# Kernel tuning notes

Measured on AMD Instinct MI355X. Metric: run time of the kernel, lower is better.

Reference implementation:

```python
import jax, jax.numpy as jnp
import numpy as np

N_NODES = 50000
N_EDGES = 800000
D_IN = 96
D_EDGE = 32
D_OUT = 96
N_TYPES = 4


def setup_inputs() -> dict:
    key = jax.random.key(0)
    k = jax.random.split(key, 6)
    x = jax.random.normal(k[0], (N_NODES, D_IN), dtype=jnp.float32)
    edge_features = jax.random.normal(k[1], (N_NODES, D_EDGE), dtype=jnp.float32)
    edge_index = jax.random.randint(k[2], (2, N_EDGES), 0, N_NODES, dtype=jnp.int32)
    edge_type = jax.random.randint(k[3], (N_EDGES,), 0, N_TYPES, dtype=jnp.int32)
    # One RelEdgeConv per relation type: Linear(D_IN + D_EDGE -> D_OUT) message fn
    scale = 1.0 / np.sqrt(D_IN + D_EDGE)
    W_msg = jax.random.uniform(k[4], (N_TYPES, D_IN + D_EDGE, D_OUT), jnp.float32, -scale, scale)
    b_msg = jax.random.uniform(k[5], (N_TYPES, D_OUT), jnp.float32, -scale, scale)
    return {"x": x, "edge_features": edge_features, "edge_index": edge_index,
            "edge_type": edge_type, "W_msg": W_msg, "b_msg": b_msg}


def reference(x, edge_features, edge_index, edge_type, W_msg, b_msg):
    # Node-level edge_features (shape[0] == N) -> per-edge relative features
    src, dst = edge_index[0], edge_index[1]
    e = jnp.abs(edge_features[src] - edge_features[dst])          # [E, De]
    feat = jnp.concatenate([x[src], e], axis=-1)                  # [E, Din+De]
    n_nodes = x.shape[0]
    n_types = W_msg.shape[0]

    def per_type(t):
        # relation mask: zero out messages for edges of other types
        mask = (edge_type == t).astype(x.dtype)[:, None]          # [E, 1]
        m = (feat @ W_msg[t] + b_msg[t]) * mask                   # [E, Dout]
        # scatter-add messages to destination nodes
        return jax.ops.segment_sum(m, dst, num_segments=n_nodes)  # [N, Dout]

    out = jnp.stack([per_type(t) for t in range(n_types)])        # [T, N, Dout]
    return out.mean(axis=0)
```

## Files before the change

kernel.cpp:

```cpp
#include <hip/hip_runtime.h>

#define E_EDGES 800000
#define NN 50000
#define D_IN 96
#define D_EDGE 32
#define D_OUT 96
#define KSUM 512
#define SSTRIDE 520
#define NBUCK 196
#define BCAP 4800
#define NCHUNK 256
#define CHE 3125
#define CHIT 13
#define BUILD_BLOCKS 512
#define SUBCAP 384

typedef __attribute__((ext_vector_type(8))) __bf16 bf16x8;
typedef __attribute__((ext_vector_type(4))) float floatx4;

__device__ __forceinline__ float lo16(unsigned int u) {
    return __builtin_bit_cast(float, u << 16);
}
__device__ __forceinline__ float hi16(unsigned int u) {
    return __builtin_bit_cast(float, u & 0xFFFF0000u);
}
__device__ __forceinline__ unsigned int pk2(float a, float b) {
    unsigned short ua = __builtin_bit_cast(unsigned short, (__bf16)a);
    unsigned short ub = __builtin_bit_cast(unsigned short, (__bf16)b);
    return (unsigned int)ua | ((unsigned int)ub << 16);
}

__global__ __launch_bounds__(256) void k_prep(const int* __restrict__ ei,
                                              const int* __restrict__ et,
                                              const float* __restrict__ x,
                                              const float* __restrict__ ef,
                                              const float* __restrict__ Wm,
                                              int* __restrict__ cursor,
                                              int* __restrict__ eb,
                                              __bf16* __restrict__ WT,
                                              unsigned int* __restrict__ xeb) {
    __shared__ int lcnt[NBUCK];
    __shared__ int lexcl[NBUCK];
    __shared__ int gb[NBUCK];
    __shared__ int tmp[256];
    __shared__ int stage[CHE];
    __shared__ int spos[CHE];
    int tid = threadIdx.x, bid = blockIdx.x;

    if (bid < NCHUNK) {
        int e0 = bid * CHE;
        for (int i = tid; i < NBUCK; i += 256) lcnt[i] = 0;
        __syncthreads();

        int pv[CHIT], br[CHIT];
#pragma unroll
        for (int it = 0; it < CHIT; it++) {
            int i = it * 256 + tid;
            br[it] = -1;
            if (i < CHE) {
                int e = e0 + i;
                int dst = ei[E_EDGES + e];
                int b = dst >> 8;
                int rank = atomicAdd(&lcnt[b], 1);
                pv[it] = (ei[e] << 6) | (et[e] << 22) | ((dst & 255) << 24);
                br[it] = rank | (b << 16);
            }
        }
        __syncthreads();
        int v = (tid < NBUCK) ? lcnt[tid] : 0;
        tmp[tid] = v; __syncthreads();
        for (int d = 1; d < 256; d <<= 1) {
            int t = (tid >= d) ? tmp[tid - d] : 0;
            __syncthreads();
            tmp[tid] += t; __syncthreads();
        }
        if (tid < NBUCK) lexcl[tid] = tmp[tid] - v;
        for (int b = tid; b < NBUCK; b += 256)
            gb[b] = lcnt[b] ? atomicAdd(&cursor[b], lcnt[b]) : 0;
        __syncthreads();
#pragma unroll
        for (int it = 0; it < CHIT; it++) {
            if (br[it] >= 0) {
                int b = br[it] >> 16, rank = br[it] & 0xFFFF;
                int lidx = lexcl[b] + rank;
                stage[lidx] = pv[it];
                int gp = gb[b] + rank;
                spos[lidx] = (gp < BCAP) ? (b * BCAP + gp) : -1;
            }
        }
        __syncthreads();
        for (int i = tid; i < CHE; i += 256) {
            int p = spos[i];
            if (p >= 0) eb[p] = stage[i];
        }
    } else {
        int b2 = bid - NCHUNK;
        int gtid = b2 * 256 + tid;
        int lane = tid & 63, w = tid >> 6;
        for (int n = b2 * 4 + w; n < NN; n += BUILD_BLOCKS * 4) {
            float2 v;
            if (lane < 48) v = *(const float2*)(x  + (size_t)n * D_IN   + 2 * lane);
            else           v = *(const float2*)(ef + (size_t)n * D_EDGE + 2 * (lane - 48));
            xeb[(size_t)n * 64 + lane] = pk2(v.x, v.y);
        }
        for (int i = gtid; i < 96 * KSUM; i += BUILD_BLOCKS * 256) {
            int n = i >> 9, k = i & 511;
            WT[n * KSUM + k] = (__bf16)Wm[(size_t)k * 96 + n];
        }
    }
}

__global__ __launch_bounds__(256) void k_fused(const int* __restrict__ cursor,
                                               const int* __restrict__ eb,
                                               const unsigned int* __restrict__ xeb,
                                               const __bf16* __restrict__ WT,
                                               const float* __restrict__ bm,
                                               float* __restrict__ out) {
    __shared__ __align__(16) __bf16 Sl[16][SSTRIDE];
    __shared__ int elist[SUBCAP];
    __shared__ int cnt64[64];
    __shared__ int base16[16], c2[16], tot16[16];

    int tid = threadIdx.x, lane = tid & 63, w = tid >> 6;
    int B = blockIdx.x >> 4, sg = blockIdx.x & 15;
    int seg = B * BCAP;
    int m = min(cursor[B], BCAP);

    if (tid < 64) cnt64[tid] = 0;
    __syncthreads();

    for (int i = tid; i < m; i += 256) {
        int p = eb[seg + i];
        unsigned int dl = ((unsigned int)p) >> 24;
        if ((int)(dl >> 4) == sg)
            atomicAdd(&cnt64[((dl & 15) << 2) | ((p >> 22) & 3)], 1);
    }
    __syncthreads();

    if (w == 0 && lane < 16) {
        int tot = cnt64[lane * 4] + cnt64[lane * 4 + 1]
                + cnt64[lane * 4 + 2] + cnt64[lane * 4 + 3];
        tot16[lane] = tot;
        int s = tot;
        for (int d = 1; d < 16; d <<= 1) {
            int t = __shfl_up(s, d, 64);
            if (lane >= d) s += t;
        }
        base16[lane] = s - tot;
        c2[lane] = s - tot;
    }
    __syncthreads();

    for (int i = tid; i < m; i += 256) {
        int p = eb[seg + i];
        unsigned int dl = ((unsigned int)p) >> 24;
        if ((int)(dl >> 4) == sg) {
            int pos = atomicAdd(&c2[dl & 15], 1);
            if (pos < SUBCAP) elist[pos] = p;
        }
    }
    __syncthreads();

    unsigned int Mmask = (lane >= 48) ? 0x7FFFFFFFu : 0xFFFFFFFFu;

#define ACCS(u, v) do {                                                        \
        float f0 = lo16(u), f1 = hi16(u);                                      \
        f0 = __builtin_bit_cast(float,                                         \
                 __builtin_bit_cast(unsigned int, f0 - e0) & Mmask);           \
        f1 = __builtin_bit_cast(float,                                         \
                 __builtin_bit_cast(unsigned int, f1 - e1) & Mmask);           \
        int sty = (__builtin_amdgcn_readfirstlane(v) >> 22) & 3;               \
        if      (sty == 0) { s0a += f0; s0b += f1; }                           \
        else if (sty == 1) { s1a += f0; s1b += f1; }                           \
        else if (sty == 2) { s2a += f0; s2b += f1; }                           \
        else               { s3a += f0; s3b += f1; }                           \
    } while (0)

    for (int j = 0; j < 4; j++) {
        int nl = w * 4 + j;
        int n = B * 256 + sg * 16 + nl;
        int num = tot16[nl], bs = base16[nl];
        float s0a = 0, s0b = 0, s1a = 0, s1b = 0,
              s2a = 0, s2b = 0, s3a = 0, s3b = 0;
        float e0 = 0.f, e1 = 0.f;
        if (lane >= 48 && num > 0) {
            unsigned int u = xeb[(size_t)n * 64 + lane];
            e0 = lo16(u); e1 = hi16(u);
        }

        int i = 0;
        for (; i + 7 < num; i += 8) {
            int v0 = elist[bs + i],     v1 = elist[bs + i + 1];
            int v2 = elist[bs + i + 2], v3 = elist[bs + i + 3];
            int v4 = elist[bs + i + 4], v5 = elist[bs + i + 5];
            int v6 = elist[bs + i + 6], v7 = elist[bs + i + 7];
            unsigned int u0 = xeb[(v0 & 0x3FFFFF) + lane];
            unsigned int u1 = xeb[(v1 & 0x3FFFFF) + lane];
            unsigned int u2 = xeb[(v2 & 0x3FFFFF) + lane];
            unsigned int u3 = xeb[(v3 & 0x3FFFFF) + lane];
            unsigned int u4 = xeb[(v4 & 0x3FFFFF) + lane];
            unsigned int u5 = xeb[(v5 & 0x3FFFFF) + lane];
            unsigned int u6 = xeb[(v6 & 0x3FFFFF) + lane];
            unsigned int u7 = xeb[(v7 & 0x3FFFFF) + lane];
            ACCS(u0, v0); ACCS(u1, v1); ACCS(u2, v2); ACCS(u3, v3);
            ACCS(u4, v4); ACCS(u5, v5); ACCS(u6, v6); ACCS(u7, v7);
        }
        for (; i < num; i++) {
            int v = elist[bs + i];
            unsigned int u = xeb[(v & 0x3FFFFF) + lane];
            ACCS(u, v);
        }

        unsigned int* sp = (unsigned int*)&Sl[nl][0];
        sp[  0 + lane] = pk2(s0a, s0b);
        sp[ 64 + lane] = pk2(s1a, s1b);
        sp[128 + lane] = pk2(s2a, s2b);
        sp[192 + lane] = pk2(s3a, s3b);
    }
#undef ACCS
    __syncthreads();

    int quad = lane >> 4, low = lane & 15;

    bf16x8 a[16];
    const __bf16* ap = &Sl[low][0] + quad * 8;
#pragma unroll
    for (int ks = 0; ks < 16; ks++) a[ks] = *(const bf16x8*)(ap + ks * 32);

    for (int ct = w; ct < 6; ct += 4) {
        floatx4 acc = {0.f, 0.f, 0.f, 0.f};
        const __bf16* bp = WT + (size_t)(ct * 16 + low) * KSUM + quad * 8;
#pragma unroll
        for (int ks = 0; ks < 16; ks++)
            acc = __builtin_amdgcn_mfma_f32_16x16x32_bf16(
                a[ks], *(const bf16x8*)(bp + ks * 32), acc, 0, 0, 0);
        int col = ct * 16 + low;
#pragma unroll
        for (int rg = 0; rg < 4; rg++) {
            int r = quad * 4 + rg;
            int g = B * 256 + sg * 16 + r;
            if (g < NN) {
                float bias = (float)cnt64[r * 4 + 0] * bm[col]
                           + (float)cnt64[r * 4 + 1] * bm[96 + col]
                           + (float)cnt64[r * 4 + 2] * bm[192 + col]
                           + (float)cnt64[r * 4 + 3] * bm[288 + col];
                out[(size_t)g * D_OUT + col] = 0.25f * (acc[rg] + bias);
            }
        }
    }
}

extern "C" void kernel_launch(void* const* d_in, const int* in_sizes, int n_in,
                              void* d_out, int out_size, void* d_ws, size_t ws_size,
                              hipStream_t stream) {
    const float* x  = (const float*)d_in[0];
    const float* ef = (const float*)d_in[1];
    const int*   ei = (const int*)d_in[2];
    const int*   et = (const int*)d_in[3];
    const float* Wm = (const float*)d_in[4];
    const float* bm = (const float*)d_in[5];
    float* out = (float*)d_out;

    int* cursor = (int*)d_ws;
    int* eb     = cursor + 256;
    __bf16* WT  = (__bf16*)(eb + NBUCK * BCAP);
    unsigned int* xeb = (unsigned int*)(WT + 96 * KSUM);

    hipMemsetAsync(cursor, 0, NBUCK * sizeof(int), stream);
    k_prep <<<NCHUNK + BUILD_BLOCKS, 256, 0, stream>>>(ei, et, x, ef, Wm,
                                                       cursor, eb, WT, xeb);
    k_fused<<<NBUCK * 16, 256, 0, stream>>>(cursor, eb, xeb, WT, bm, out);
}
```

Measured before the change: 205.6 us.

## Use 64-node buckets so each fused block reads only its own edges

Changes bucketing from 256-node buckets (196 buckets, each scanned by 16 blocks) to 64-node buckets (782 buckets, one block each). The fused kernel loads its bucket once into shared memory, histograms by node and type, and processes four 16-node chunks in sequence. This removes the 16x redundant scanning of each bucket's edge list. The prep kernel also drops its shared-memory staging and prefix scan and writes edges straight to global, which makes those writes less coalesced. The trade-offs are fewer fused blocks, larger shared-memory use per block, and a per-bucket capacity of 1216 that could overflow on skewed inputs.

After: 208.4 us. No clear change (+1.4%).

```diff
diff --git a/kernel.cpp b/kernel.cpp
--- a/kernel.cpp
+++ b/kernel.cpp
@@ -7,13 +7,12 @@
 #define D_OUT 96
 #define KSUM 512
 #define SSTRIDE 520
-#define NBUCK 196
-#define BCAP 4800
+#define NB2 782
+#define BCAP2 1216
 #define NCHUNK 256
 #define CHE 3125
 #define CHIT 13
 #define BUILD_BLOCKS 512
-#define SUBCAP 384
 
 typedef __attribute__((ext_vector_type(8))) __bf16 bf16x8;
 typedef __attribute__((ext_vector_type(4))) float floatx4;
@@ -39,17 +38,13 @@
                                               int* __restrict__ eb,
                                               __bf16* __restrict__ WT,
                                               unsigned int* __restrict__ xeb) {
-    __shared__ int lcnt[NBUCK];
-    __shared__ int lexcl[NBUCK];
-    __shared__ int gb[NBUCK];
-    __shared__ int tmp[256];
-    __shared__ int stage[CHE];
-    __shared__ int spos[CHE];
+    __shared__ int lcnt[NB2];
+    __shared__ int gb[NB2];
     int tid = threadIdx.x, bid = blockIdx.x;
 
     if (bid < NCHUNK) {
         int e0 = bid * CHE;
-        for (int i = tid; i < NBUCK; i += 256) lcnt[i] = 0;
+        for (int i = tid; i < NB2; i += 256) lcnt[i] = 0;
         __syncthreads();
 
         int pv[CHIT], br[CHIT];
@@ -60,38 +55,23 @@
             if (i < CHE) {
                 int e = e0 + i;
                 int dst = ei[E_EDGES + e];
-                int b = dst >> 8;
+                int b = dst >> 6;
                 int rank = atomicAdd(&lcnt[b], 1);
-                pv[it] = (ei[e] << 6) | (et[e] << 22) | ((dst & 255) << 24);
+                pv[it] = (ei[e] << 6) | (et[e] << 22) | ((dst & 63) << 24);
                 br[it] = rank | (b << 16);
             }
         }
         __syncthreads();
-        int v = (tid < NBUCK) ? lcnt[tid] : 0;
-        tmp[tid] = v; __syncthreads();
-        for (int d = 1; d < 256; d <<= 1) {
-            int t = (tid >= d) ? tmp[tid - d] : 0;
-            __syncthreads();
-            tmp[tid] += t; __syncthreads();
-        }
-        if (tid < NBUCK) lexcl[tid] = tmp[tid] - v;
-        for (int b = tid; b < NBUCK; b += 256)
+        for (int b = tid; b < NB2; b += 256)
             gb[b] = lcnt[b] ? atomicAdd(&cursor[b], lcnt[b]) : 0;
         __syncthreads();
 #pragma unroll
         for (int it = 0; it < CHIT; it++) {
             if (br[it] >= 0) {
                 int b = br[it] >> 16, rank = br[it] & 0xFFFF;
-                int lidx = lexcl[b] + rank;
-                stage[lidx] = pv[it];
-                int gp = gb[b] + rank;
-                spos[lidx] = (gp < BCAP) ? (b * BCAP + gp) : -1;
-            }
-        }
-        __syncthreads();
-        for (int i = tid; i < CHE; i += 256) {
-            int p = spos[i];
-            if (p >= 0) eb[p] = stage[i];
+                int pos = gb[b] + rank;
+                if (pos < BCAP2) eb[b * BCAP2 + pos] = pv[it];
+            }
         }
     } else {
         int b2 = bid - NCHUNK;
@@ -116,48 +96,41 @@
                                                const __bf16* __restrict__ WT,
                                                const float* __restrict__ bm,
                                                float* __restrict__ out) {
+    __shared__ int ecopy[BCAP2];
+    __shared__ int elist[BCAP2];
+    __shared__ int h[256], hbase[256], c2[256];
     __shared__ __align__(16) __bf16 Sl[16][SSTRIDE];
-    __shared__ int elist[SUBCAP];
-    __shared__ int cnt64[64];
-    __shared__ int base16[16], c2[16], tot16[16];
 
     int tid = threadIdx.x, lane = tid & 63, w = tid >> 6;
-    int B = blockIdx.x >> 4, sg = blockIdx.x & 15;
-    int seg = B * BCAP;
-    int m = min(cursor[B], BCAP);
-
-    if (tid < 64) cnt64[tid] = 0;
+    int B = blockIdx.x;
+    int seg = B * BCAP2;
+    int m = min(cursor[B], BCAP2);
+
+    h[tid] = 0;
     __syncthreads();
 
     for (int i = tid; i < m; i += 256) {
         int p = eb[seg + i];
-        unsigned int dl = ((unsigned int)p) >> 24;
-        if ((int)(dl >> 4) == sg)
-            atomicAdd(&cnt64[((dl & 15) << 2) | ((p >> 22) & 3)], 1);
-    }
-    __syncthreads();
-
-    if (w == 0 && lane < 16) {
-        int tot = cnt64[lane * 4] + cnt64[lane * 4 + 1]
-                + cnt64[lane * 4 + 2] + cnt64[lane * 4 + 3];
-        tot16[lane] = tot;
-        int s = tot;
-        for (int d = 1; d < 16; d <<= 1) {
-            int t = __shfl_up(s, d, 64);
-            if (lane >= d) s += t;
-        }
-        base16[lane] = s - tot;
-        c2[lane] = s - tot;
-    }
+        ecopy[i] = p;
+        atomicAdd(&h[(p >> 22) & 255], 1);
+    }
+    __syncthreads();
+
+    int v = h[tid];
+    c2[tid] = v; __syncthreads();
+    for (int d = 1; d < 256; d <<= 1) {
+        int t = (tid >= d) ? c2[tid - d] : 0;
+        __syncthreads();
+        c2[tid] += t; __syncthreads();
+    }
+    hbase[tid] = c2[tid] - v;
+    c2[tid] = c2[tid] - v;
     __syncthreads();
 
     for (int i = tid; i < m; i += 256) {
-        int p = eb[seg + i];
-        unsigned int dl = ((unsigned int)p) >> 24;
-        if ((int)(dl >> 4) == sg) {
-            int pos = atomicAdd(&c2[dl & 15], 1);
-            if (pos < SUBCAP) elist[pos] = p;
-        }
+        int p = ecopy[i];
+        int pos = atomicAdd(&c2[(p >> 22) & 255], 1);
+        elist[pos] = p;
     }
     __syncthreads();
 
@@ -176,78 +149,84 @@
         else               { s3a += f0; s3b += f1; }                           \
     } while (0)
 
-    for (int j = 0; j < 4; j++) {
-        int nl = w * 4 + j;
-        int n = B * 256 + sg * 16 + nl;
-        int num = tot16[nl], bs = base16[nl];
-        float s0a = 0, s0b = 0, s1a = 0, s1b = 0,
-              s2a = 0, s2b = 0, s3a = 0, s3b = 0;
-        float e0 = 0.f, e1 = 0.f;
-        if (lane >= 48 && num > 0) {
-            unsigned int u = xeb[(size_t)n * 64 + lane];
-            e0 = lo16(u); e1 = hi16(u);
-        }
-
-        int i = 0;
-        for (; i + 7 < num; i += 8) {
-            int v0 = elist[bs + i],     v1 = elist[bs + i + 1];
-            int v2 = elist[bs + i + 2], v3 = elist[bs + i + 3];
-            int v4 = elist[bs + i + 4], v5 = elist[bs + i + 5];
-            int v6 = elist[bs + i + 6], v7 = elist[bs + i + 7];
-            unsigned int u0 = xeb[(v0 & 0x3FFFFF) + lane];
-            unsigned int u1 = xeb[(v1 & 0x3FFFFF) + lane];
-            unsigned int u2 = xeb[(v2 & 0x3FFFFF) + lane];
-            unsigned int u3 = xeb[(v3 & 0x3FFFFF) + lane];
-            unsigned int u4 = xeb[(v4 & 0x3FFFFF) + lane];
-            unsigned int u5 = xeb[(v5 & 0x3FFFFF) + lane];
-            unsigned int u6 = xeb[(v6 & 0x3FFFFF) + lane];
-            unsigned int u7 = xeb[(v7 & 0x3FFFFF) + lane];
-            ACCS(u0, v0); ACCS(u1, v1); ACCS(u2, v2); ACCS(u3, v3);
-            ACCS(u4, v4); ACCS(u5, v5); ACCS(u6, v6); ACCS(u7, v7);
-        }
-        for (; i < num; i++) {
-            int v = elist[bs + i];
-            unsigned int u = xeb[(v & 0x3FFFFF) + lane];
-            ACCS(u, v);
-        }
-
-        unsigned int* sp = (unsigned int*)&Sl[nl][0];
-        sp[  0 + lane] = pk2(s0a, s0b);
-        sp[ 64 + lane] = pk2(s1a, s1b);
-        sp[128 + lane] = pk2(s2a, s2b);
-        sp[192 + lane] = pk2(s3a, s3b);
+    int quad = lane >> 4, low = lane & 15;
+
+    for (int c4 = 0; c4 < 4; c4++) {
+        for (int j = 0; j < 4; j++) {
+            int lr = w * 4 + j;
+            int nl = c4 * 16 + lr;
+            int n = B * 64 + nl;
+            int bs = hbase[nl * 4];
+            int num = h[nl * 4] + h[nl * 4 + 1] + h[nl * 4 + 2] + h[nl * 4 + 3];
+            float s0a = 0, s0b = 0, s1a = 0, s1b = 0,
+                  s2a = 0, s2b = 0, s3a = 0, s3b = 0;
+            float e0 = 0.f, e1 = 0.f;
+            if (lane >= 48 && num > 0) {
+                unsigned int u = xeb[(size_t)n * 64 + lane];
+                e0 = lo16(u); e1 = hi16(u);
+            }
+
+            int i = 0;
+            for (; i + 7 < num; i += 8) {
+                int v0 = elist[bs + i],     v1 = elist[bs + i + 1];
+                int v2 = elist[bs + i + 2], v3 = elist[bs + i + 3];
+                int v4 = elist[bs + i + 4], v5 = elist[bs + i + 5];
+                int v6 = elist[bs + i + 6], v7 = elist[bs + i + 7];
+                unsigned int u0 = xeb[(v0 & 0x3FFFFF) + lane];
+                unsigned int u1 = xeb[(v1 & 0x3FFFFF) + lane];
+                unsigned int u2 = xeb[(v2 & 0x3FFFFF) + lane];
+                unsigned int u3 = xeb[(v3 & 0x3FFFFF) + lane];
+                unsigned int u4 = xeb[(v4 & 0x3FFFFF) + lane];
+                unsigned int u5 = xeb[(v5 & 0x3FFFFF) + lane];
+                unsigned int u6 = xeb[(v6 & 0x3FFFFF) + lane];
+                unsigned int u7 = xeb[(v7 & 0x3FFFFF) + lane];
+                ACCS(u0, v0); ACCS(u1, v1); ACCS(u2, v2); ACCS(u3, v3);
+                ACCS(u4, v4); ACCS(u5, v5); ACCS(u6, v6); ACCS(u7, v7);
+            }
+            for (; i < num; i++) {
+                int vv = elist[bs + i];
+                unsigned int u = xeb[(vv & 0x3FFFFF) + lane];
+                ACCS(u, vv);
+            }
+
+            unsigned int* sp = (unsigned int*)&Sl[lr][0];
+            sp[  0 + lane] = pk2(s0a, s0b);
+            sp[ 64 + lane] = pk2(s1a, s1b);
+            sp[128 + lane] = pk2(s2a, s2b);
+            sp[192 + lane] = pk2(s3a, s3b);
+        }
+        __syncthreads();
+
+        bf16x8 a[16];
+        const __bf16* ap = &Sl[low][0] + quad * 8;
+#pragma unroll
+        for (int ks = 0; ks < 16; ks++) a[ks] = *(const bf16x8*)(ap + ks * 32);
+
+        for (int ct = w; ct < 6; ct += 4) {
+            floatx4 acc = {0.f, 0.f, 0.f, 0.f};
+            const __bf16* bp = WT + (size_t)(ct * 16 + low) * KSUM + quad * 8;
+#pragma unroll
+            for (int ks = 0; ks < 16; ks++)
+                acc = __builtin_amdgcn_mfma_f32_16x16x32_bf16(
+                    a[ks], *(const bf16x8*)(bp + ks * 32), acc, 0, 0, 0);
+            int col = ct * 16 + low;
+#pragma unroll
+            for (int rg = 0; rg < 4; rg++) {
+                int r = quad * 4 + rg;
+                int nl = c4 * 16 + r;
+                int g = B * 64 + nl;
+                if (g < NN) {
+                    float bias = (float)h[nl * 4 + 0] * bm[col]
+                               + (float)h[nl * 4 + 1] * bm[96 + col]
+                               + (float)h[nl * 4 + 2] * bm[192 + col]
+                               + (float)h[nl * 4 + 3] * bm[288 + col];
+                    out[(size_t)g * D_OUT + col] = 0.25f * (acc[rg] + bias);
+                }
+            }
+        }
+        __syncthreads();
     }
 #undef ACCS
-    __syncthreads();
-
-    int quad = lane >> 4, low = lane & 15;
-
-    bf16x8 a[16];
-    const __bf16* ap = &Sl[low][0] + quad * 8;
-#pragma unroll
-    for (int ks = 0; ks < 16; ks++) a[ks] = *(const bf16x8*)(ap + ks * 32);
-
-    for (int ct = w; ct < 6; ct += 4) {
-        floatx4 acc = {0.f, 0.f, 0.f, 0.f};
-        const __bf16* bp = WT + (size_t)(ct * 16 + low) * KSUM + quad * 8;
-#pragma unroll
-        for (int ks = 0; ks < 16; ks++)
-            acc = __builtin_amdgcn_mfma_f32_16x16x32_bf16(
-                a[ks], *(const bf16x8*)(bp + ks * 32), acc, 0, 0, 0);
-        int col = ct * 16 + low;
-#pragma unroll
-        for (int rg = 0; rg < 4; rg++) {
-            int r = quad * 4 + rg;
-            int g = B * 256 + sg * 16 + r;
-            if (g < NN) {
-                float bias = (float)cnt64[r * 4 + 0] * bm[col]
-                           + (float)cnt64[r * 4 + 1] * bm[96 + col]
-                           + (float)cnt64[r * 4 + 2] * bm[192 + col]
-                           + (float)cnt64[r * 4 + 3] * bm[288 + col];
-                out[(size_t)g * D_OUT + col] = 0.25f * (acc[rg] + bias);
-            }
-        }
-    }
 }
 
 extern "C" void kernel_launch(void* const* d_in, const int* in_sizes, int n_in,
@@ -262,12 +241,12 @@
     float* out = (float*)d_out;
 
     int* cursor = (int*)d_ws;
-    int* eb     = cursor + 256;
-    __bf16* WT  = (__bf16*)(eb + NBUCK * BCAP);
+    int* eb     = cursor + 1024;
+    __bf16* WT  = (__bf16*)(eb + NB2 * BCAP2);
     unsigned int* xeb = (unsigned int*)(WT + 96 * KSUM);
 
-    hipMemsetAsync(cursor, 0, NBUCK * sizeof(int), stream);
+    hipMemsetAsync(cursor, 0, NB2 * sizeof(int), stream);
     k_prep <<<NCHUNK + BUILD_BLOCKS, 256, 0, stream>>>(ei, et, x, ef, Wm,
                                                        cursor, eb, WT, xeb);
-    k_fused<<<NBUCK * 16, 256, 0, stream>>>(cursor, eb, xeb, WT, bm, out);
-}
+    k_fused<<<NB2, 256, 0, stream>>>(cursor, eb, xeb, WT, bm, out);
+}
```
